# Kernel optimization log

Hardware: AMD Instinct MI355X
Metric: run time of the kernel (lower is better)

Reference implementation:

```python
import jax, jax.numpy as jnp
import numpy as np

N, E, C, ED = 50000, 800000, 128, 16
NEG_SLOPE = 0.2


def setup_inputs() -> dict:
    key = jax.random.key(0)
    ks = jax.random.split(key, 18)
    inp = {
        "h": jax.random.normal(ks[0], (N, C), jnp.float32),
        "edge_index": jax.random.randint(ks[1], (2, E), 0, N),
        "edge_attr": jax.random.normal(ks[2], (E, ED), jnp.float32),
        "reducible": jax.random.randint(ks[3], (N,), 0, 2) > 0,
    }
    names = ["W", "att_src", "att_dst", "W_edge", "att_edge", "W_res", "bias"]
    shapes = [(C, C), (C,), (C,), (ED, C), (C,), (C, C), (C,)]
    i = 4
    for pre in ["red_", "irr_"]:
        for n, sh in zip(names, shapes):
            inp[pre + n] = jax.random.normal(ks[i], sh, jnp.float32) * 0.05
            i += 1
    return inp


def _gat_conv(h, src, dst, edge_attr, W, att_src, att_dst, W_edge, att_edge, W_res, bias):
    """PyG GATConv (heads=1, residual=True, add_self_loops=True, fill_value='mean')."""
    n = h.shape[0]
    # self-loop edge_attr = mean of incoming edge_attr per node (0 if none)
    sum_attr = jax.ops.segment_sum(edge_attr, dst, num_segments=n)
    cnt = jax.ops.segment_sum(jnp.ones((edge_attr.shape[0],), edge_attr.dtype), dst, num_segments=n)
    mean_attr = sum_attr / jnp.maximum(cnt, 1.0)[:, None]
    loop = jnp.arange(n)
    s = jnp.concatenate([src, loop])   # [E+N]
    d = jnp.concatenate([dst, loop])   # [E+N]
    ea = jnp.concatenate([edge_attr, mean_attr], axis=0)  # [E+N, ED]
    x = h @ W                              # [N, C]
    a_src = x @ att_src                    # [N]
    a_dst = x @ att_dst                    # [N]
    a_edge = (ea @ W_edge) @ att_edge      # [E+N]
    alpha = jax.nn.leaky_relu(a_src[s] + a_dst[d] + a_edge, NEG_SLOPE)
    # per-destination softmax (every node has a self-loop -> denom > 0)
    m = jax.ops.segment_max(alpha, d, num_segments=n)
    ex = jnp.exp(alpha - m[d])
    denom = jax.ops.segment_sum(ex, d, num_segments=n)
    w = ex / denom[d]                      # [E+N]
    out = jax.ops.segment_sum(w[:, None] * x[s], d, num_segments=n)  # [N, C]
    return out + h @ W_res + bias


def reference(h, edge_index, edge_attr, reducible,
              red_W, red_att_src, red_att_dst, red_W_edge, red_att_edge, red_W_res, red_bias,
              irr_W, irr_att_src, irr_att_dst, irr_W_edge, irr_att_edge, irr_W_res, irr_bias):
    src, dst = edge_index[0], edge_index[1]
    out_r = _gat_conv(h, src, dst, edge_attr, red_W, red_att_src, red_att_dst,
                      red_W_edge, red_att_edge, red_W_res, red_bias)
    out_i = _gat_conv(h, src, dst, edge_attr, irr_W, irr_att_src, irr_att_dst,
                      irr_W_edge, irr_att_edge, irr_W_res, irr_bias)
    return jax.nn.relu(jnp.where(reducible[:, None], out_r, out_i))
```

## Files before the change

kernel.cpp:

```cpp
#include <hip/hip_runtime.h>
#include <hip/hip_bf16.h>

#define CDIM 128
#define EDIM 16
#define NEG_SLOPE 0.2f

typedef __attribute__((ext_vector_type(8))) short bf16x8;
typedef __attribute__((ext_vector_type(4))) float f32x4;
typedef __attribute__((ext_vector_type(2))) float f32x2;
typedef unsigned int uint;
typedef unsigned short ushort;

__device__ __forceinline__ ushort f2bf(float f) {
    uint u = __float_as_uint(f);
    return (ushort)((u + 0x7fffu + ((u >> 16) & 1u)) >> 16);
}
__device__ __forceinline__ uint packbf(float lo, float hi) {
    return ((uint)f2bf(hi) << 16) | (uint)f2bf(lo);
}
__device__ __forceinline__ float bflo(uint w) { return __uint_as_float(w << 16); }
__device__ __forceinline__ float bfhi(uint w) { return __uint_as_float(w & 0xffff0000u); }

__device__ __forceinline__ bool redtest(const void* red, int i, int notInt, int notFloat) {
    if (!notInt)        return ((const int*)red)[i] != 0;
    else if (!notFloat) return ((const float*)red)[i] != 0.f;
    else                return ((const unsigned char*)red)[i] != 0;
}

__global__ __launch_bounds__(256) void bcatwe_kernel(const float* __restrict__ Wr, const float* __restrict__ Wi,
                              const float* __restrict__ Wrr, const float* __restrict__ Wri,
                              ushort* __restrict__ BT,
                              const float* __restrict__ WeR, const float* __restrict__ aeR,
                              const float* __restrict__ WeI, const float* __restrict__ aeI,
                              float* __restrict__ we,
                              int* __restrict__ cnt8, int* __restrict__ flags,
                              const float* __restrict__ h, ushort* __restrict__ hbf,
                              int N8, int n4) {
    int gtid = blockIdx.x * 256 + threadIdx.x;
    for (int i = gtid; i < N8; i += gridDim.x * 256) cnt8[i] = 0;
    if (gtid == 0) { flags[0] = 0; flags[1] = 0; flags[2] = 0; }
    if (gtid < n4) {
        f32x4 v = __builtin_nontemporal_load((const f32x4*)h + gtid);
        uint2 o;
        o.x = packbf(v.x, v.y);
        o.y = packbf(v.z, v.w);
        ((uint2*)hbf)[gtid] = o;
    }
    if (blockIdx.x < 256) {
        int idx = blockIdx.x * 256 + threadIdx.x;
        int c = idx >> 7, k = idx & 127;
        const float* srcm;
        if (c < 128)      srcm = Wr;
        else if (c < 256) srcm = Wi;
        else if (c < 384) srcm = Wrr;
        else              srcm = Wri;
        BT[idx] = f2bf(srcm[k * 128 + (c & 127)]);
    } else if (blockIdx.x == 256) {
        int lane = threadIdx.x;
        if (lane < 16) {
            float s = 0.f;
            for (int c = 0; c < CDIM; ++c) s += WeR[lane * CDIM + c] * aeR[c];
            we[lane] = s;
        } else if (lane < 32) {
            int j = lane - 16;
            float s = 0.f;
            for (int c = 0; c < CDIM; ++c) s += WeI[j * CDIM + c] * aeI[c];
            we[16 + j] = s;
        }
    }
}

__global__ __launch_bounds__(256) void prep_kernel(const uint* __restrict__ red, int nwords,
                                                   int* __restrict__ flags,
                                                   const int* __restrict__ dst, int* __restrict__ cnt8,
                                                   int* __restrict__ rank,
                                                   const float* __restrict__ ea, const float* __restrict__ we,
                                                   uint* __restrict__ escal4,
                                                   int N, int E) {
    int i = blockIdx.x * 256 + threadIdx.x;
    int c = blockIdx.x & 7;
    if (i < nwords) {
        uint w = red[i];
        bool isInt = (w <= 1u);
        bool isFloat = (w == 0u) || (w == 0x3f800000u);
        if (!isInt) atomicOr(&flags[0], 1);
        if (!isFloat) atomicOr(&flags[1], 1);
    }
    if (i < E) {
        int d = dst[i];
        int rk = atomicAdd(&cnt8[c * N + d], 1);
        __builtin_nontemporal_store(rk | (c << 28), rank + i);
        const f32x4* row = (const f32x4*)(ea + (size_t)i * EDIM);
        const float4* we4 = (const float4*)we;
        float er = 0.f, ei = 0.f;
#pragma unroll
        for (int q = 0; q < 4; ++q) {
            f32x4 v = __builtin_nontemporal_load(row + q);
            float4 wr = we4[q], wi = we4[4 + q];
            er += v.x * wr.x + v.y * wr.y + v.z * wr.z + v.w * wr.w;
            ei += v.x * wi.x + v.y * wi.y + v.z * wi.z + v.w * wi.w;
        }
        __builtin_nontemporal_store(packbf(er, ei), escal4 + i);
    }
}

__global__ __launch_bounds__(256) void gemm_dots(const ushort* __restrict__ A,
                                                 const ushort* __restrict__ BT,
                                                 ushort* __restrict__ C,
                                                 const float* __restrict__ attsr, const float* __restrict__ attdr,
                                                 const float* __restrict__ attsi, const float* __restrict__ attdi,
                                                 float* __restrict__ asr, float* __restrict__ adr,
                                                 float* __restrict__ asi, float* __restrict__ adi,
                                                 int M) {
    __shared__ ushort As[128 * 128];
    __shared__ ushort Bs[128 * 128];
    __shared__ float dots[4][128];
    int t = threadIdx.x;
    int lane = t & 63, wv = t >> 6;
    int rb = blockIdx.x * 128;

    if (t < 128) { dots[0][t] = 0.f; dots[1][t] = 0.f; dots[2][t] = 0.f; dots[3][t] = 0.f; }

    int rsub = wv * 4 + (lane >> 4);
    int c0 = lane & 15;
#pragma unroll
    for (int p = 0; p < 8; ++p) {
        int row = p * 16 + rsub;
        int chunk = c0 ^ (row & 7);
        int gra = rb + row; if (gra > M - 1) gra = M - 1;
        const ushort* ga = A + (size_t)gra * 128 + chunk * 8;
        __builtin_amdgcn_global_load_lds(
            (const __attribute__((address_space(1))) void*)ga,
            (__attribute__((address_space(3))) void*)((char*)As + p * 4096 + wv * 1024),
            16, 0, 0);
    }

    int wr = wv >> 1, wc = wv & 1;
    int l15 = lane & 15, l4 = lane >> 4;
    const char* Ab = (const char*)As;
    const char* Bb = (const char*)Bs;

    for (int s = 0; s < 4; ++s) {
#pragma unroll
        for (int p = 0; p < 8; ++p) {
            int row = p * 16 + rsub;
            int chunk = c0 ^ (row & 7);
            const ushort* gb = BT + (size_t)(s * 128 + row) * 128 + chunk * 8;
            __builtin_amdgcn_global_load_lds(
                (const __attribute__((address_space(1))) void*)gb,
                (__attribute__((address_space(3))) void*)((char*)Bs + p * 4096 + wv * 1024),
                16, 0, 0);
        }
        __syncthreads();

        f32x4 acc[4][4];
#pragma unroll
        for (int i = 0; i < 4; ++i)
#pragma unroll
            for (int j = 0; j < 4; ++j) acc[i][j] = (f32x4){0.f, 0.f, 0.f, 0.f};

#pragma unroll
        for (int ks = 0; ks < 4; ++ks) {
            bf16x8 a[4], b[4];
#pragma unroll
            for (int f = 0; f < 4; ++f) {
                int row = wr * 64 + f * 16 + l15;
                int ch = (ks * 4 + l4) ^ (row & 7);
                a[f] = *(const bf16x8*)(Ab + row * 256 + ch * 16);
                int col = wc * 64 + f * 16 + l15;
                int ch2 = (ks * 4 + l4) ^ (col & 7);
                b[f] = *(const bf16x8*)(Bb + col * 256 + ch2 * 16);
            }
#pragma unroll
            for (int i = 0; i < 4; ++i)
#pragma unroll
                for (int j = 0; j < 4; ++j)
                    acc[i][j] = __builtin_amdgcn_mfma_f32_16x16x32_bf16(a[i], b[j], acc[i][j], 0, 0, 0);
        }

        if (s < 2) {
            const float* attS = s ? attsi : attsr;
            const float* attD = s ? attdi : attdr;
            float aS[4], aD[4];
#pragma unroll
            for (int j = 0; j < 4; ++j) {
                int c = wc * 64 + j * 16 + l15;
                aS[j] = attS[c]; aD[j] = attD[c];
            }
#pragma unroll
            for (int i = 0; i < 4; ++i)
#pragma unroll
                for (int rr = 0; rr < 4; ++rr) {
                    float ps = 0.f, pd = 0.f;
#pragma unroll
                    for (int j = 0; j < 4; ++j) {
                        float v = acc[i][j][rr];
                        ps += v * aS[j]; pd += v * aD[j];
                    }
#pragma unroll
                    for (int d = 1; d < 16; d <<= 1) {
                        ps += __shfl_xor(ps, d); pd += __shfl_xor(pd, d);
                    }
                    if (l15 == 0) {
                        int row = wr * 64 + i * 16 + l4 * 4 + rr;
                        atomicAdd(&dots[s * 2 + 0][row], ps);
                        atomicAdd(&dots[s * 2 + 1][row], pd);
                    }
                }
        }

#pragma unroll
        for (int i = 0; i < 4; ++i) {
            int rl = wr * 64 + i * 16 + l4 * 4;
#pragma unroll
            for (int j = 0; j < 4; ++j) {
                int col = s * 128 + wc * 64 + j * 16 + l15;
#pragma unroll
                for (int r = 0; r < 4; ++r) {
                    int gr = rb + rl + r;
                    if (gr < M) C[(size_t)gr * 512 + col] = f2bf(acc[i][j][r]);
                }
            }
        }
        __syncthreads();
    }

    if (t < 128) {
        int gr = rb + t;
        if (gr < M) {
            asr[gr] = dots[0][t]; adr[gr] = dots[1][t];
            asi[gr] = dots[2][t]; adi[gr] = dots[3][t];
        }
    }
}

__global__ __launch_bounds__(256) void scanA_kernel(int* __restrict__ cnt8,
                                                    int* __restrict__ offA,
                                                    int* __restrict__ bsum,
                                                    int* __restrict__ doneCnt,
                                                    int n, int nb) {
    __shared__ int wsum[4];
    __shared__ int s_last;
    int t = threadIdx.x, lane = t & 63, wid = t >> 6;
    if (t == 0) s_last = 0;
    int i0 = blockIdx.x * 1024 + t * 4;
    int v[4];
#pragma unroll
    for (int j = 0; j < 4; ++j) {
        int d = i0 + j;
        int tot = 0;
        if (d < n) {
#pragma unroll
            for (int x = 0; x < 8; ++x) {
                int cv = cnt8[x * n + d];
                cnt8[x * n + d] = tot;
                tot += cv;
            }
        }
        v[j] = tot;
    }
    int s = v[0] + v[1] + v[2] + v[3];
    int incl = s;
#pragma unroll
    for (int d = 1; d < 64; d <<= 1) { int u = __shfl_up(incl, d); if (lane >= d) incl += u; }
    if (lane == 63) wsum[wid] = incl;
    __syncthreads();
    int wpre = 0;
    for (int w = 0; w < wid; ++w) wpre += wsum[w];
    int run = wpre + incl - s;
#pragma unroll
    for (int j = 0; j < 4; ++j) {
        int i = i0 + j;
        if (i < n) offA[i] = run;
        run += v[j];
    }
    if (t == 255) {
        bsum[blockIdx.x] = wpre + incl;
        __threadfence();
        int old = atomicAdd(doneCnt, 1);
        if (old == (int)gridDim.x - 1) s_last = 1;
    }
    __syncthreads();
    if (s_last && t < 64) {
        __threadfence();
        int v2 = (t < nb) ? bsum[t] : 0;
        int incl2 = v2;
#pragma unroll
        for (int d = 1; d < 64; d <<= 1) { int u = __shfl_up(incl2, d); if (t >= d) incl2 += u; }
        if (t < nb) bsum[t] = incl2 - v2;
    }
}

__global__ __launch_bounds__(256) void scatter_kernel(
    const int* __restrict__ src, const int* __restrict__ dst,
    const int* __restrict__ rank, const uint* __restrict__ escal4,
    const void* __restrict__ red, const int* __restrict__ flags,
    const int* __restrict__ offA, const int* __restrict__ bsum,
    const int* __restrict__ cnt8,
    uint* __restrict__ csr, int N, int E) {
    int e = blockIdx.x * 256 + threadIdx.x;
    if (e >= E) return;
    int s = __builtin_nontemporal_load(src + e);
    int d = __builtin_nontemporal_load(dst + e);
    uint ee = __builtin_nontemporal_load(escal4 + e);
    int rkw = __builtin_nontemporal_load(rank + e);
    int c = ((uint)rkw) >> 28;
    int rk = rkw & 0x0fffffff;
    int notInt = flags[0], notFloat = flags[1];
    bool rr = redtest(red, d, notInt, notFloat);
    uint evb = rr ? (ee & 0xffffu) : (ee >> 16);
    int off = offA[d] + bsum[d >> 10] + cnt8[c * N + d];
    csr[off + rk] = (uint)s | (evb << 16);
}

__global__ __launch_bounds__(256) void node_kernel(
    const ushort* __restrict__ xcat,
    const float* __restrict__ adst_r, const float* __restrict__ adst_i,
    const float* __restrict__ asrc_r, const float* __restrict__ asrc_i,
    const void* __restrict__ red, const int* __restrict__ flags,
    const int* __restrict__ offA, const int* __restrict__ bsum,
    const uint* __restrict__ csr,
    const float* __restrict__ bias_r, const float* __restrict__ bias_i,
    float* __restrict__ out, int n, int E) {
    __shared__ uint2 buf[4][64];
    int wv = threadIdx.x >> 6, lane = threadIdx.x & 63;
    int node = blockIdx.x * 4 + wv;
    if (node >= n) return;

    int notInt = flags[0], notFloat = flags[1];
    bool r = redtest(red, node, notInt, notFloat);

    const float* asrc = r ? asrc_r : asrc_i;
    float adst = (r ? adst_r : adst_i)[node];
    uint vsel = r ? 0u : 256u;
    int b0 = offA[node] + bsum[node >> 10];
    int b1 = (node + 1 < n) ? (offA[node + 1] + bsum[(node + 1) >> 10]) : E;
    int k = b1 - b0;
    const char* xb = (const char*)xcat;
    uint lane4 = lane * 4;

    float denom_l = 0.f, sumE = 0.f;
    float2 acca = make_float2(0.f, 0.f), accb = make_float2(0.f, 0.f);

    for (int base = b0; base < b1; base += 64) {
        int j = base + lane;
        float ex = 0.f; uint soff = 0;
        if (j < b1) {
            uint rec = __builtin_nontemporal_load(csr + j);
            uint s = rec & 0xffffu;
            float ev = bfhi(rec);
            sumE += ev;
            soff = s * 1024u + vsel;
            float a = asrc[s] + ev + adst;
            float al = (a >= 0.f) ? a : NEG_SLOPE * a;
            ex = __expf(fminf(al, 60.f));
            denom_l += ex;
        }
        buf[wv][lane] = make_uint2(__float_as_uint(ex), soff);
        __builtin_amdgcn_wave_barrier();
        int cc = min(64, b1 - base);
        int ccp = (cc + 7) & ~7;
        for (int tq = 0; tq < ccp; tq += 8) {
            uint2 u[8];
#pragma unroll
            for (int q = 0; q < 8; ++q) u[q] = buf[wv][tq + q];
            uint v[8];
#pragma unroll
            for (int q = 0; q < 8; ++q) v[q] = *(const uint*)(xb + u[q].y + lane4);
#pragma unroll
            for (int q = 0; q < 4; ++q) {
                float w = __uint_as_float(u[q].x);
                acca.x += w * bflo(v[q]); acca.y += w * bfhi(v[q]);
            }
#pragma unroll
            for (int q = 4; q < 8; ++q) {
                float w = __uint_as_float(u[q].x);
                accb.x += w * bflo(v[q]); accb.y += w * bfhi(v[q]);
            }
        }
        __builtin_amdgcn_wave_barrier();
    }
    float acc0 = acca.x + accb.x, acc1 = acca.y + accb.y;

#pragma unroll
    for (int d = 32; d; d >>= 1) {
        sumE += __shfl_xor(sumE, d);
        denom_l += __shfl_xor(denom_l, d);
    }

    float eself = sumE / fmaxf((float)k, 1.f);
    float a = asrc[node] + adst + eself;
    float aself = (a >= 0.f) ? a : NEG_SLOPE * a;
    float exl = __expf(fminf(aself, 60.f));
    float denom = denom_l + exl;
    uint voff = (uint)node * 1024u + vsel;
    uint vsw = *(const uint*)(xb + voff + lane4);
    acc0 += exl * bflo(vsw);
    acc1 += exl * bfhi(vsw);

    float inv = 1.f / denom;
    uint roff = (uint)node * 1024u + (r ? 512u : 768u);
    uint bw = *(const uint*)(xb + roff + lane4);
    float2 bi2 = ((const float2*)(r ? bias_r : bias_i))[lane];
    f32x2 o;
    o.x = fmaxf(acc0 * inv + bflo(bw) + bi2.x, 0.f);
    o.y = fmaxf(acc1 * inv + bfhi(bw) + bi2.y, 0.f);
    __builtin_nontemporal_store(o, ((f32x2*)out) + (size_t)node * 64 + lane);
}

extern "C" void kernel_launch(void* const* d_in, const int* in_sizes, int n_in,
                              void* d_out, int out_size, void* d_ws, size_t ws_size,
                              hipStream_t stream) {
    const float* h          = (const float*)d_in[0];
    const int*   edge_index = (const int*)d_in[1];
    const float* edge_attr  = (const float*)d_in[2];
    const void*  reducible  = d_in[3];
    const float* red_W      = (const float*)d_in[4];
    const float* red_att_src= (const float*)d_in[5];
    const float* red_att_dst= (const float*)d_in[6];
    const float* red_W_edge = (const float*)d_in[7];
    const float* red_att_edge=(const float*)d_in[8];
    const float* red_W_res  = (const float*)d_in[9];
    const float* red_bias   = (const float*)d_in[10];
    const float* irr_W      = (const float*)d_in[11];
    const float* irr_att_src= (const float*)d_in[12];
    const float* irr_att_dst= (const float*)d_in[13];
    const float* irr_W_edge = (const float*)d_in[14];
    const float* irr_att_edge=(const float*)d_in[15];
    const float* irr_W_res  = (const float*)d_in[16];
    const float* irr_bias   = (const float*)d_in[17];

    const int N = in_sizes[0] / CDIM;
    const int E = in_sizes[1] / 2;
    const int* src = edge_index;
    const int* dst = edge_index + E;
    const int nb = (N + 1023) / 1024;
    const int n4 = N * 128 / 4;

    float* out = (float*)d_out;

    size_t cur = 0;
    auto alloc = [&](size_t bytes) { size_t p = cur; cur = (cur + bytes + 255) & ~(size_t)255; return p; };
    char* ws = (char*)d_ws;
    size_t o_xcat  = alloc((size_t)N * 512 * 2);
    size_t o_hbf   = alloc((size_t)N * 128 * 2);
    size_t o_bcat  = alloc(512 * 128 * 2);
    size_t o_we    = alloc(256);
    size_t o_asr   = alloc((size_t)N * 4);
    size_t o_adr   = alloc((size_t)N * 4);
    size_t o_asi   = alloc((size_t)N * 4);
    size_t o_adi   = alloc((size_t)N * 4);
    size_t o_flags = alloc(256);
    size_t o_cnt8  = alloc((size_t)N * 8 * 4);
    size_t o_offA  = alloc((size_t)N * 4);
    size_t o_bsum  = alloc((size_t)(nb + 1) * 4);
    size_t o_rank  = alloc((size_t)E * 4);
    size_t o_escal = alloc((size_t)E * 4);
    size_t o_csr   = alloc((size_t)E * 4);
    if (cur > ws_size) return;

    ushort* xcat = (ushort*)(ws + o_xcat);
    ushort* hbf  = (ushort*)(ws + o_hbf);
    ushort* bcat = (ushort*)(ws + o_bcat);
    float* we    = (float*)(ws + o_we);
    float* asr   = (float*)(ws + o_asr);
    float* adr   = (float*)(ws + o_adr);
    float* asi   = (float*)(ws + o_asi);
    float* adi   = (float*)(ws + o_adi);
    int*   flags = (int*)(ws + o_flags);
    int*   cnt8  = (int*)(ws + o_cnt8);
    int*   offA  = (int*)(ws + o_offA);
    int*   bsum  = (int*)(ws + o_bsum);
    int*   rank  = (int*)(ws + o_rank);
    uint*  escal4= (uint*)(ws + o_escal);
    uint*  csr   = (uint*)(ws + o_csr);

    int N8 = N * 8;
    int bgrid = (n4 + 255) / 256;
    if (bgrid < 257) bgrid = 257;
    bcatwe_kernel<<<bgrid, 256, 0, stream>>>(red_W, irr_W, red_W_res, irr_W_res, bcat,
                                             red_W_edge, red_att_edge, irr_W_edge, irr_att_edge, we,
                                             cnt8, flags, h, hbf, N8, n4);

    int nwords = N / 4;
    prep_kernel<<<(E + 255) / 256, 256, 0, stream>>>((const uint*)reducible, nwords, flags,
                                                     dst, cnt8, rank, edge_attr, we, escal4,
                                                     N, E);

    gemm_dots<<<(N + 127) / 128, 256, 0, stream>>>(hbf, bcat, xcat,
                                                   red_att_src, red_att_dst,
                                                   irr_att_src, irr_att_dst,
                                                   asr, adr, asi, adi, N);

    scanA_kernel<<<nb, 256, 0, stream>>>(cnt8, offA, bsum, flags + 2, N, nb);

    scatter_kernel<<<(E + 255) / 256, 256, 0, stream>>>(src, dst, rank, escal4,
                                                        reducible, flags, offA, bsum, cnt8,
                                                        csr, N, E);

    node_kernel<<<(N + 3) / 4, 256, 0, stream>>>(xcat, adr, adi, asr, asi,
                                                 reducible, flags, offA, bsum, csr,
                                                 red_bias, irr_bias, out, N, E);
}
```

Measured before the change: 149.1 us.

## Fuse edge prep kernel into GEMM launch as extra blocks

Combines prep_kernel and gemm_dots into a single launch, where blocks past the GEMM grid perform the edge ranking, flag checks and edge scalar computation. This removes one kernel launch and the serialization between two independent stages, letting memory-bound prep overlap with the GEMM. The cost is that the prep blocks now carry the GEMM's large shared-memory allocation, which limits how many of them can be resident per CU.

```diff
diff --git a/kernel.cpp b/kernel.cpp
--- a/kernel.cpp
+++ b/kernel.cpp
@@ -70,54 +70,54 @@
     }
 }
 
-__global__ __launch_bounds__(256) void prep_kernel(const uint* __restrict__ red, int nwords,
-                                                   int* __restrict__ flags,
-                                                   const int* __restrict__ dst, int* __restrict__ cnt8,
-                                                   int* __restrict__ rank,
-                                                   const float* __restrict__ ea, const float* __restrict__ we,
-                                                   uint* __restrict__ escal4,
-                                                   int N, int E) {
-    int i = blockIdx.x * 256 + threadIdx.x;
-    int c = blockIdx.x & 7;
-    if (i < nwords) {
-        uint w = red[i];
-        bool isInt = (w <= 1u);
-        bool isFloat = (w == 0u) || (w == 0x3f800000u);
-        if (!isInt) atomicOr(&flags[0], 1);
-        if (!isFloat) atomicOr(&flags[1], 1);
-    }
-    if (i < E) {
-        int d = dst[i];
-        int rk = atomicAdd(&cnt8[c * N + d], 1);
-        __builtin_nontemporal_store(rk | (c << 28), rank + i);
-        const f32x4* row = (const f32x4*)(ea + (size_t)i * EDIM);
-        const float4* we4 = (const float4*)we;
-        float er = 0.f, ei = 0.f;
-#pragma unroll
-        for (int q = 0; q < 4; ++q) {
-            f32x4 v = __builtin_nontemporal_load(row + q);
-            float4 wr = we4[q], wi = we4[4 + q];
-            er += v.x * wr.x + v.y * wr.y + v.z * wr.z + v.w * wr.w;
-            ei += v.x * wi.x + v.y * wi.y + v.z * wi.z + v.w * wi.w;
-        }
-        __builtin_nontemporal_store(packbf(er, ei), escal4 + i);
-    }
-}
-
-__global__ __launch_bounds__(256) void gemm_dots(const ushort* __restrict__ A,
-                                                 const ushort* __restrict__ BT,
-                                                 ushort* __restrict__ C,
-                                                 const float* __restrict__ attsr, const float* __restrict__ attdr,
-                                                 const float* __restrict__ attsi, const float* __restrict__ attdi,
-                                                 float* __restrict__ asr, float* __restrict__ adr,
-                                                 float* __restrict__ asi, float* __restrict__ adi,
-                                                 int M) {
+__global__ __launch_bounds__(256) void gemmprep_kernel(
+    const ushort* __restrict__ A, const ushort* __restrict__ BT, ushort* __restrict__ C,
+    const float* __restrict__ attsr, const float* __restrict__ attdr,
+    const float* __restrict__ attsi, const float* __restrict__ attdi,
+    float* __restrict__ asr, float* __restrict__ adr,
+    float* __restrict__ asi, float* __restrict__ adi, int M, int GB,
+    const uint* __restrict__ red, int nwords, int* __restrict__ flags,
+    const int* __restrict__ dst, int* __restrict__ cnt8, int* __restrict__ rank,
+    const float* __restrict__ ea, const float* __restrict__ we,
+    uint* __restrict__ escal4, int N, int E) {
     __shared__ ushort As[128 * 128];
     __shared__ ushort Bs[128 * 128];
     __shared__ float dots[4][128];
+    int bid = blockIdx.x;
     int t = threadIdx.x;
+
+    if (bid >= GB) {
+        int pb = bid - GB;
+        int i = pb * 256 + t;
+        int c = pb & 7;
+        if (i < nwords) {
+            uint w = red[i];
+            bool isInt = (w <= 1u);
+            bool isFloat = (w == 0u) || (w == 0x3f800000u);
+            if (!isInt) atomicOr(&flags[0], 1);
+            if (!isFloat) atomicOr(&flags[1], 1);
+        }
+        if (i < E) {
+            int d = dst[i];
+            int rk = atomicAdd(&cnt8[c * N + d], 1);
+            __builtin_nontemporal_store(rk | (c << 28), rank + i);
+            const f32x4* row = (const f32x4*)(ea + (size_t)i * EDIM);
+            const float4* we4 = (const float4*)we;
+            float er = 0.f, ei = 0.f;
+#pragma unroll
+            for (int q = 0; q < 4; ++q) {
+                f32x4 v = __builtin_nontemporal_load(row + q);
+                float4 wr = we4[q], wi = we4[4 + q];
+                er += v.x * wr.x + v.y * wr.y + v.z * wr.z + v.w * wr.w;
+                ei += v.x * wi.x + v.y * wi.y + v.z * wi.z + v.w * wi.w;
+            }
+            __builtin_nontemporal_store(packbf(er, ei), escal4 + i);
+        }
+        return;
+    }
+
     int lane = t & 63, wv = t >> 6;
-    int rb = blockIdx.x * 128;
+    int rb = bid * 128;
 
     if (t < 128) { dots[0][t] = 0.f; dots[1][t] = 0.f; dots[2][t] = 0.f; dots[3][t] = 0.f; }
 
@@ -483,14 +483,14 @@
                                              cnt8, flags, h, hbf, N8, n4);
 
     int nwords = N / 4;
-    prep_kernel<<<(E + 255) / 256, 256, 0, stream>>>((const uint*)reducible, nwords, flags,
-                                                     dst, cnt8, rank, edge_attr, we, escal4,
-                                                     N, E);
-
-    gemm_dots<<<(N + 127) / 128, 256, 0, stream>>>(hbf, bcat, xcat,
-                                                   red_att_src, red_att_dst,
-                                                   irr_att_src, irr_att_dst,
-                                                   asr, adr, asi, adi, N);
+    int GB = (N + 127) / 128;
+    int PB = (E + 255) / 256;
+    gemmprep_kernel<<<GB + PB, 256, 0, stream>>>(hbf, bcat, xcat,
+                                                 red_att_src, red_att_dst,
+                                                 irr_att_src, irr_att_dst,
+                                                 asr, adr, asi, adi, N, GB,
+                                                 (const uint*)reducible, nwords, flags,
+                                                 dst, cnt8, rank, edge_attr, we, escal4, N, E);
 
     scanA_kernel<<<nb, 256, 0, stream>>>(cnt8, offA, bsum, flags + 2, N, nb);
 
```

Result: faster. 141.7 us (-5.0%).
